# Performance work log

Measured on AMD Instinct MI355X. Metric: run time of the kernel, lower is better.

Reference implementation:

```python
import jax, jax.numpy as jnp
import numpy as np

B, L, S, DE, D = 16, 2048, 1024, 512, 256
VOP, NSIL, A, NN = 64, 8, 64, 100000


def setup_inputs() -> dict:
    key = jax.random.key(0)
    ks = jax.random.split(key, 11)
    return {
        "encoded_sentence_tokens": jax.random.normal(ks[0], (B, S, DE), jnp.float32),
        "encoded_stack_nodes": jax.random.normal(ks[1], (NN, D), jnp.float32),
        "silent_embeddings": jax.random.normal(ks[2], (NSIL, D), jnp.float32),
        "op_embedding": jax.random.normal(ks[3], (VOP, D), jnp.float32) * 0.02,
        "w_shift": jax.random.normal(ks[4], (DE, D), jnp.float32) / np.sqrt(DE).astype(np.float32),
        "b_shift": jnp.zeros((D,), jnp.float32),
        "op_tokens": jax.random.randint(ks[5], (B, L), 0, VOP),
        "arg_idx": jax.random.randint(ks[6], (B, L), 0, NSIL + A),
        "shift_idx": jax.random.randint(ks[7], (B, L), 0, S),
        "item_type": jax.random.randint(ks[8], (B, L), 0, 3),
        "avail_nodes": jax.random.randint(ks[9], (B, L, A), 0, NN),
    }


def reference(encoded_sentence_tokens, encoded_stack_nodes, silent_embeddings,
              op_embedding, w_shift, b_shift,
              op_tokens, arg_idx, shift_idx, item_type, avail_nodes):
    # Operation embeddings: [B, L, D]
    emb_ops = op_embedding[op_tokens]

    # Shift-arg embeddings: gather sentence encodings per (b, l), then linear. [B, L, D]
    gathered_sent = jnp.take_along_axis(
        encoded_sentence_tokens, shift_idx[:, :, None], axis=1)  # [B, L, DE]
    emb_shift = jnp.einsum('ble,ed->bld', gathered_sent, w_shift) + b_shift

    # Argument embeddings: choice index < NSIL -> silent embedding, else stack node.
    # Equivalent to concat([silent, available_node_embs], axis=2)[arg_idx] without
    # materializing the [B, L, NSIL+A, D] choice tensor.
    is_silent = arg_idx < NSIL                                    # [B, L]
    silent_sel = silent_embeddings[jnp.clip(arg_idx, 0, NSIL - 1)]  # [B, L, D]
    node_pos = jnp.clip(arg_idx - NSIL, 0, A - 1)                 # [B, L]
    node_ids = jnp.take_along_axis(avail_nodes, node_pos[:, :, None], axis=2)[..., 0]
    node_sel = encoded_stack_nodes[node_ids]                      # [B, L, D]
    emb_args = jnp.where(is_silent[:, :, None], silent_sel, node_sel)

    # combine_embeddings: positional masks align, so it's a 3-way select by type.
    t = item_type[:, :, None]
    result = jnp.where(t == 0, emb_ops,
             jnp.where(t == 1, emb_args,
             jnp.where(t == 2, emb_shift, jnp.zeros_like(emb_ops))))
    return result
```

## Files before the change

### kernel.cpp

```cpp
#include <hip/hip_runtime.h>

#define B_    16
#define L_    2048
#define S_    1024
#define DE_   512
#define D_    256
#define NSIL_ 8
#define A_    64
#define NR_   (B_ * L_)

#define BM 64
#define BN 256
#define BK 64
#define NGEMM (NR_ / BM)
#define NT01  256

typedef __attribute__((ext_vector_type(8))) short  short8;
typedef __attribute__((ext_vector_type(4))) float  f32x4;

__device__ __forceinline__ unsigned short f2bf(float f) {
    unsigned int x = __builtin_bit_cast(unsigned int, f);
    x += 0x7fffu + ((x >> 16) & 1u);
    return (unsigned short)(x >> 16);
}

__global__ __launch_bounds__(256) void srse_wt(
    const float* __restrict__ w, unsigned short* __restrict__ wT)
{
    __shared__ float tile[64][65];
    const int t  = threadIdx.x;
    const int kb = (blockIdx.x >> 2) << 6;
    const int nb = (blockIdx.x & 3) << 6;

    #pragma unroll
    for (int p = 0; p < 4; ++p) {
        const int id = p * 256 + t;
        const int k  = id >> 4;
        const int n4 = id & 15;
        const float4 v = *(const float4*)(w + (size_t)(kb + k) * D_ + nb + n4 * 4);
        tile[k][n4 * 4 + 0] = v.x;
        tile[k][n4 * 4 + 1] = v.y;
        tile[k][n4 * 4 + 2] = v.z;
        tile[k][n4 * 4 + 3] = v.w;
    }
    __syncthreads();

    const int n  = t >> 2;
    const int kq = t & 3;
    short8 o0, o1;
    #pragma unroll
    for (int j = 0; j < 8; ++j) o0[j] = (short)f2bf(tile[kq * 16 + j][n]);
    #pragma unroll
    for (int j = 0; j < 8; ++j) o1[j] = (short)f2bf(tile[kq * 16 + 8 + j][n]);
    *(short8*)(wT + (size_t)(nb + n) * DE_ + kb + kq * 16)     = o0;
    *(short8*)(wT + (size_t)(nb + n) * DE_ + kb + kq * 16 + 8) = o1;
}

__global__ __launch_bounds__(512) void srse_mega(
    const float*          __restrict__ sent,
    const unsigned short* __restrict__ wT,
    const float*          __restrict__ bsh,
    const float*          __restrict__ op_emb,
    const float*          __restrict__ silent,
    const float*          __restrict__ nodes,
    const int*            __restrict__ op_tokens,
    const int*            __restrict__ arg_idx,
    const int*            __restrict__ shift_idx,
    const int*            __restrict__ item_type,
    const int*            __restrict__ avail,
    float*                __restrict__ out)
{
    __shared__ alignas(16) unsigned short As[BM * BK];
    __shared__ alignas(16) unsigned short Bs[BN * BK];

    const int t    = threadIdx.x;
    const int lane = t & 63;
    const int wid  = t >> 6;

    if (blockIdx.x < NGEMM) {
        const int gm0 = blockIdx.x * BM;

        const int srow = t >> 3;
        const int k8   = t & 7;
        const int orow = gm0 + srow;
        const int sb   = orow >> 11;
        const float* abase = sent + ((size_t)((sb << 10) + shift_idx[orow]) * DE_) + k8 * 8;
        const int awidx = ((srow * BK + k8 * 8) ^ ((srow & 7) << 3));

        const int wm = wid & 1;
        const int wn = wid >> 1;
        const int fr = lane & 15;
        const int fq = lane >> 4;

        f32x4 acc[2][4] = {};

        for (int k0 = 0; k0 < DE_; k0 += BK) {
            {
                const float4 a0 = *(const float4*)(abase + k0);
                const float4 a1 = *(const float4*)(abase + k0 + 4);
                short8 v;
                v[0] = f2bf(a0.x); v[1] = f2bf(a0.y); v[2] = f2bf(a0.z); v[3] = f2bf(a0.w);
                v[4] = f2bf(a1.x); v[5] = f2bf(a1.y); v[6] = f2bf(a1.z); v[7] = f2bf(a1.w);
                *(short8*)(As + awidx) = v;
            }
            #pragma unroll
            for (int p = 0; p < 4; ++p) {
                const int id = p * 512 + t;
                const int n  = id >> 3;
                const int kb8 = id & 7;
                short8 v = *(const short8*)(wT + (size_t)n * DE_ + k0 + kb8 * 8);
                *(short8*)(Bs + ((n * BK + kb8 * 8) ^ ((n & 7) << 3))) = v;
            }
            __syncthreads();

            #pragma unroll
            for (int ks = 0; ks < 2; ++ks) {
                short8 af[2], bfr[4];
                #pragma unroll
                for (int mf = 0; mf < 2; ++mf) {
                    const int row = wm * 32 + mf * 16 + fr;
                    af[mf] = *(const short8*)(As + ((row * BK + ks * 32 + fq * 8) ^ ((row & 7) << 3)));
                }
                #pragma unroll
                for (int nf = 0; nf < 4; ++nf) {
                    const int n = wn * 64 + nf * 16 + fr;
                    bfr[nf] = *(const short8*)(Bs + ((n * BK + ks * 32 + fq * 8) ^ ((n & 7) << 3)));
                }
                #pragma unroll
                for (int mf = 0; mf < 2; ++mf)
                    #pragma unroll
                    for (int nf = 0; nf < 4; ++nf)
                        acc[mf][nf] = __builtin_amdgcn_mfma_f32_16x16x32_bf16(
                            af[mf], bfr[nf], acc[mf][nf], 0, 0, 0);
            }
            __syncthreads();
        }

        int t2m[2][4];
        #pragma unroll
        for (int mf = 0; mf < 2; ++mf)
            #pragma unroll
            for (int r = 0; r < 4; ++r)
                t2m[mf][r] = item_type[gm0 + wm * 32 + mf * 16 + fq * 4 + r];

        #pragma unroll
        for (int nf = 0; nf < 4; ++nf) {
            const int col = wn * 64 + nf * 16 + fr;
            const float bval = bsh[col];
            #pragma unroll
            for (int mf = 0; mf < 2; ++mf) {
                #pragma unroll
                for (int r = 0; r < 4; ++r) {
                    if (t2m[mf][r] == 2) {
                        const int row = gm0 + wm * 32 + mf * 16 + fq * 4 + r;
                        out[(size_t)row * D_ + col] = acc[mf][nf][r] + bval;
                    }
                }
            }
        }
    } else {
        const int bid2 = blockIdx.x - NGEMM;
        const int r0w  = bid2 * 128 + wid * 16;

        #pragma unroll
        for (int b8 = 0; b8 < 2; ++b8) {
            const int r0 = r0w + b8 * 8;
            const float* src[8];
            int tt8[8];
            #pragma unroll
            for (int i = 0; i < 8; ++i) {
                const int row = r0 + i;
                const int tt  = item_type[row];
                tt8[i] = tt;
                const int a = arg_idx[row];
                int np = a - NSIL_;
                np = np < 0 ? 0 : (np > A_ - 1 ? A_ - 1 : np);
                const float* s0 = op_emb + (size_t)op_tokens[row] * D_;
                const float* s1 = (a < NSIL_)
                                  ? silent + (size_t)a * D_
                                  : nodes + (size_t)avail[(size_t)row * A_ + np] * D_;
                src[i] = (tt == 0) ? s0 : s1;
            }
            float4 v[8];
            #pragma unroll
            for (int i = 0; i < 8; ++i)
                v[i] = *(const float4*)(src[i] + lane * 4);
            #pragma unroll
            for (int i = 0; i < 8; ++i)
                if (tt8[i] != 2)
                    *(float4*)(out + (size_t)(r0 + i) * D_ + lane * 4) = v[i];
        }
    }
}

extern "C" void kernel_launch(void* const* d_in, const int* in_sizes, int n_in,
                              void* d_out, int out_size, void* d_ws, size_t ws_size,
                              hipStream_t stream) {
    const float* sent      = (const float*)d_in[0];
    const float* nodes     = (const float*)d_in[1];
    const float* silent    = (const float*)d_in[2];
    const float* op_emb    = (const float*)d_in[3];
    const float* w         = (const float*)d_in[4];
    const float* bsh       = (const float*)d_in[5];
    const int*   op_tokens = (const int*)d_in[6];
    const int*   arg_idx   = (const int*)d_in[7];
    const int*   shift_idx = (const int*)d_in[8];
    const int*   item_type = (const int*)d_in[9];
    const int*   avail     = (const int*)d_in[10];
    float*       out       = (float*)d_out;

    unsigned short* wT = (unsigned short*)d_ws;

    srse_wt<<<32, 256, 0, stream>>>(w, wT);

    srse_mega<<<NGEMM + NT01, 512, 0, stream>>>(
        sent, wT, bsh, op_emb, silent, nodes,
        op_tokens, arg_idx, shift_idx, item_type, avail, out);
}
```

Measured before the change: 210.7 us.

## Compact shift rows into a worklist so GEMM only processes type-2 rows

```diff
diff --git a/kernel.cpp b/kernel.cpp
--- a/kernel.cpp
+++ b/kernel.cpp
@@ -15,6 +15,9 @@
 #define NGEMM (NR_ / BM)
 #define NT01  256
 
+#define NPREP_WT 32
+#define NPREP_CP (NR_ / 256)
+
 typedef __attribute__((ext_vector_type(8))) short  short8;
 typedef __attribute__((ext_vector_type(4))) float  f32x4;
 
@@ -24,36 +27,51 @@
     return (unsigned short)(x >> 16);
 }
 
-__global__ __launch_bounds__(256) void srse_wt(
-    const float* __restrict__ w, unsigned short* __restrict__ wT)
+__global__ __launch_bounds__(256) void srse_prep(
+    const float* __restrict__ w, unsigned short* __restrict__ wT,
+    const int* __restrict__ item_type, int* __restrict__ cnt,
+    int* __restrict__ wl)
 {
-    __shared__ float tile[64][65];
-    const int t  = threadIdx.x;
-    const int kb = (blockIdx.x >> 2) << 6;
-    const int nb = (blockIdx.x & 3) << 6;
-
-    #pragma unroll
-    for (int p = 0; p < 4; ++p) {
-        const int id = p * 256 + t;
-        const int k  = id >> 4;
-        const int n4 = id & 15;
-        const float4 v = *(const float4*)(w + (size_t)(kb + k) * D_ + nb + n4 * 4);
-        tile[k][n4 * 4 + 0] = v.x;
-        tile[k][n4 * 4 + 1] = v.y;
-        tile[k][n4 * 4 + 2] = v.z;
-        tile[k][n4 * 4 + 3] = v.w;
+    const int t = threadIdx.x;
+    if (blockIdx.x < NPREP_WT) {
+        __shared__ float tile[64][65];
+        const int kb = (blockIdx.x >> 2) << 6;
+        const int nb = (blockIdx.x & 3) << 6;
+
+        #pragma unroll
+        for (int p = 0; p < 4; ++p) {
+            const int id = p * 256 + t;
+            const int k  = id >> 4;
+            const int n4 = id & 15;
+            const float4 v = *(const float4*)(w + (size_t)(kb + k) * D_ + nb + n4 * 4);
+            tile[k][n4 * 4 + 0] = v.x;
+            tile[k][n4 * 4 + 1] = v.y;
+            tile[k][n4 * 4 + 2] = v.z;
+            tile[k][n4 * 4 + 3] = v.w;
+        }
+        __syncthreads();
+
+        const int n  = t >> 2;
+        const int kq = t & 3;
+        short8 o0, o1;
+        #pragma unroll
+        for (int j = 0; j < 8; ++j) o0[j] = (short)f2bf(tile[kq * 16 + j][n]);
+        #pragma unroll
+        for (int j = 0; j < 8; ++j) o1[j] = (short)f2bf(tile[kq * 16 + 8 + j][n]);
+        *(short8*)(wT + (size_t)(nb + n) * DE_ + kb + kq * 16)     = o0;
+        *(short8*)(wT + (size_t)(nb + n) * DE_ + kb + kq * 16 + 8) = o1;
+    } else {
+        const int row  = (blockIdx.x - NPREP_WT) * 256 + t;
+        const int lane = t & 63;
+        const bool is2 = (item_type[row] == 2);
+        const unsigned long long mask = __ballot(is2);
+        int base = 0;
+        if (lane == 0 && mask)
+            base = atomicAdd(cnt, (int)__popcll(mask));
+        base = __shfl(base, 0);
+        if (is2)
+            wl[base + (int)__popcll(mask & ((1ull << lane) - 1ull))] = row;
     }
-    __syncthreads();
-
-    const int n  = t >> 2;
-    const int kq = t & 3;
-    short8 o0, o1;
-    #pragma unroll
-    for (int j = 0; j < 8; ++j) o0[j] = (short)f2bf(tile[kq * 16 + j][n]);
-    #pragma unroll
-    for (int j = 0; j < 8; ++j) o1[j] = (short)f2bf(tile[kq * 16 + 8 + j][n]);
-    *(short8*)(wT + (size_t)(nb + n) * DE_ + kb + kq * 16)     = o0;
-    *(short8*)(wT + (size_t)(nb + n) * DE_ + kb + kq * 16 + 8) = o1;
 }
 
 __global__ __launch_bounds__(512) void srse_mega(
@@ -68,6 +86,8 @@
     const int*            __restrict__ shift_idx,
     const int*            __restrict__ item_type,
     const int*            __restrict__ avail,
+    const int*            __restrict__ cnt,
+    const int*            __restrict__ wl,
     float*                __restrict__ out)
 {
     __shared__ alignas(16) unsigned short As[BM * BK];
@@ -78,13 +98,17 @@
     const int wid  = t >> 6;
 
     if (blockIdx.x < NGEMM) {
-        const int gm0 = blockIdx.x * BM;
+        const int n2 = *cnt;
+        const int i0 = blockIdx.x * BM;
+        if (i0 >= n2) return;
+        const int m = (n2 - i0 < BM) ? (n2 - i0) : BM;
 
         const int srow = t >> 3;
         const int k8   = t & 7;
-        const int orow = gm0 + srow;
-        const int sb   = orow >> 11;
-        const float* abase = sent + ((size_t)((sb << 10) + shift_idx[orow]) * DE_) + k8 * 8;
+        const int scl  = (srow < m) ? srow : m - 1;
+        const int arow = wl[i0 + scl];
+        const int sb   = arow >> 11;
+        const float* abase = sent + ((size_t)((sb << 10) + shift_idx[arow]) * DE_) + k8 * 8;
         const int awidx = ((srow * BK + k8 * 8) ^ ((srow & 7) << 3));
 
         const int wm = wid & 1;
@@ -105,8 +129,8 @@
             }
             #pragma unroll
             for (int p = 0; p < 4; ++p) {
-                const int id = p * 512 + t;
-                const int n  = id >> 3;
+                const int id  = p * 512 + t;
+                const int n   = id >> 3;
                 const int kb8 = id & 7;
                 short8 v = *(const short8*)(wT + (size_t)n * DE_ + k0 + kb8 * 8);
                 *(short8*)(Bs + ((n * BK + kb8 * 8) ^ ((n & 7) << 3))) = v;
@@ -136,27 +160,24 @@
             __syncthreads();
         }
 
-        int t2m[2][4];
+        int orow[2][4];
         #pragma unroll
         for (int mf = 0; mf < 2; ++mf)
             #pragma unroll
-            for (int r = 0; r < 4; ++r)
-                t2m[mf][r] = item_type[gm0 + wm * 32 + mf * 16 + fq * 4 + r];
+            for (int r = 0; r < 4; ++r) {
+                const int lrow = wm * 32 + mf * 16 + fq * 4 + r;
+                orow[mf][r] = wl[i0 + ((lrow < m) ? lrow : m - 1)];
+            }
 
         #pragma unroll
         for (int nf = 0; nf < 4; ++nf) {
             const int col = wn * 64 + nf * 16 + fr;
             const float bval = bsh[col];
             #pragma unroll
-            for (int mf = 0; mf < 2; ++mf) {
-                #pragma unroll
-                for (int r = 0; r < 4; ++r) {
-                    if (t2m[mf][r] == 2) {
-                        const int row = gm0 + wm * 32 + mf * 16 + fq * 4 + r;
-                        out[(size_t)row * D_ + col] = acc[mf][nf][r] + bval;
-                    }
-                }
-            }
+            for (int mf = 0; mf < 2; ++mf)
+                #pragma unroll
+                for (int r = 0; r < 4; ++r)
+                    out[(size_t)orow[mf][r] * D_ + col] = acc[mf][nf][r] + bval;
         }
     } else {
         const int bid2 = blockIdx.x - NGEMM;
@@ -179,7 +200,7 @@
                 const float* s1 = (a < NSIL_)
                                   ? silent + (size_t)a * D_
                                   : nodes + (size_t)avail[(size_t)row * A_ + np] * D_;
-                src[i] = (tt == 0) ? s0 : s1;
+                src[i] = (tt == 1) ? s1 : s0;
             }
             float4 v[8];
             #pragma unroll
@@ -209,11 +230,15 @@
     const int*   avail     = (const int*)d_in[10];
     float*       out       = (float*)d_out;
 
-    unsigned short* wT = (unsigned short*)d_ws;
-
-    srse_wt<<<32, 256, 0, stream>>>(w, wT);
+    unsigned short* wT  = (unsigned short*)d_ws;
+    int*            cnt = (int*)((char*)d_ws + 262144);
+    int*            wl  = (int*)((char*)d_ws + 262144 + 256);
+
+    hipMemsetAsync(cnt, 0, sizeof(int), stream);
+
+    srse_prep<<<NPREP_WT + NPREP_CP, 256, 0, stream>>>(w, wT, item_type, cnt, wl);
 
     srse_mega<<<NGEMM + NT01, 512, 0, stream>>>(
         sent, wT, bsh, op_emb, silent, nodes,
-        op_tokens, arg_idx, shift_idx, item_type, avail, out);
-}
+        op_tokens, arg_idx, shift_idx, item_type, avail, cnt, wl, out);
+}
```

Result: no change. 207.6 us (-1.5%).
